# Optimization experiments

Hardware: AMD Instinct MI355X
Metric: run time of the kernel (lower is better)

Reference implementation:

```python
import jax, jax.numpy as jnp
import numpy as np

N_NODES = 100000
N_EDGES = 1600000
IN_C = 64
HID = 64
OUT_C = 40


def setup_inputs() -> dict:
    key = jax.random.key(0)
    ks = jax.random.split(key, 12)
    def lin_init(k, fan_in, shape):
        bound = 1.0 / np.sqrt(fan_in)
        return jax.random.uniform(k, shape, jnp.float32, -bound, bound)
    x0 = jax.random.normal(ks[0], (N_NODES, IN_C), jnp.float32)
    edge_index = jax.random.randint(ks[1], (2, N_EDGES), 0, N_NODES, jnp.int64)
    return {
        "x0": x0,
        "edge_index": edge_index,
        "W1": lin_init(ks[2], IN_C, (HID, IN_C)),
        "b1": lin_init(ks[3], IN_C, (HID,)),
        "Wr1": lin_init(ks[4], IN_C, (HID, IN_C)),
        "br1": lin_init(ks[5], IN_C, (HID,)),
        "W2": lin_init(ks[6], HID, (HID, HID)),
        "b2": lin_init(ks[7], HID, (HID,)),
        "Wr2": lin_init(ks[8], HID, (HID, HID)),
        "br2": lin_init(ks[9], HID, (HID,)),
        "Wl": lin_init(ks[10], 2 * HID, (OUT_C, 2 * HID)),
        "bl": lin_init(ks[11], 2 * HID, (OUT_C,)),
    }


def _norm_weights(row, col, num_nodes):
    # symmetric degree normalization: d^-1/2[row] * d^-1/2[col]
    ones = jnp.ones(row.shape[0], jnp.float32)
    deg = jax.ops.segment_sum(ones, row, num_segments=num_nodes)
    dis = jnp.where(deg > 0, jax.lax.rsqrt(jnp.maximum(deg, 1.0)) * jnp.where(deg > 0, 1.0, 0.0), 0.0)
    dis = jnp.where(deg > 0, deg ** -0.5, 0.0)
    return dis[row] * dis[col]


def _bigraph_conv(x, row, col, w, W, b, Wr, br, num_nodes):
    h = x @ W.T + b                                    # [N, out]
    msg = w[:, None] * h[col]                          # gather + scale, [E, out]
    agg = jax.ops.segment_sum(msg, row, num_segments=num_nodes)
    return agg + x @ Wr.T + br


def reference(x0, edge_index, W1, b1, Wr1, br1, W2, b2, Wr2, br2, Wl, bl):
    num_nodes = x0.shape[0]
    row, col = edge_index[0], edge_index[1]
    w = _norm_weights(row, col, num_nodes)
    x1 = jax.nn.relu(_bigraph_conv(x0, row, col, w, W1, b1, Wr1, br1, num_nodes))
    x2 = jax.nn.relu(_bigraph_conv(x1, row, col, w, W2, b2, Wr2, br2, num_nodes))
    x = jnp.concatenate([x1, x2], axis=-1)
    logits = x @ Wl.T + bl
    return jax.nn.log_softmax(logits, axis=-1)
```

## Files before the change

### kernel.cpp

```cpp
#include <hip/hip_runtime.h>
#include <math.h>


typedef unsigned short u16;
typedef unsigned int   u32;

#define BROWS 512
#define BIN_CHUNK 8192
#define CAPB 12288

__device__ __forceinline__ u16 f2bf(float f) {
  u32 u = __float_as_uint(f);
  u32 r = u + 0x7fffu + ((u >> 16) & 1u);
  return (u16)(r >> 16);
}
__device__ __forceinline__ float bf2f(u16 h) {
  return __uint_as_float(((u32)h) << 16);
}

__global__ __launch_bounds__(1024) void k_binA(
    const int* __restrict__ row, const int* __restrict__ col,
    unsigned* __restrict__ bCnt, unsigned* __restrict__ pairs,
    int nE, int NB, int capA)
{
  __shared__ unsigned buf[BIN_CHUNK];
  __shared__ unsigned cnt[16][256];
  __shared__ unsigned base[256], gb[256], tot[256], sc[256];
  const int t = threadIdx.x;
  const int wave = t >> 6, lane = t & 63;
  const int tb = blockIdx.x * BIN_CHUNK;

  for (int i = t; i < 16 * 256; i += 1024) ((unsigned*)cnt)[i] = 0;
  __syncthreads();

  unsigned pk[8];
  unsigned short po[8];
  short bk[8];
#pragma unroll
  for (int j = 0; j < 8; ++j) {
    int i = tb + j * 1024 + t;
    if (i < nE) {
      int r = row[i], c = col[i];
      int b = r >> 9;
      pk[j] = ((unsigned)(r & (BROWS - 1)) << 17) | (unsigned)c;
      bk[j] = (short)b;
      po[j] = (unsigned short)atomicAdd(&cnt[wave][b], 1u);
    } else bk[j] = -1;
  }
  __syncthreads();

  if (t < 256) {
    unsigned run = 0;
#pragma unroll
    for (int w = 0; w < 16; ++w) {
      unsigned c = cnt[w][t];
      cnt[w][t] = run;
      run += c;
    }
    tot[t] = run;
    sc[t] = run;
  }
  __syncthreads();
  for (int off = 1; off < 256; off <<= 1) {
    unsigned v = 0;
    if (t < 256 && t >= off) v = sc[t - off];
    __syncthreads();
    if (t < 256) sc[t] += v;
    __syncthreads();
  }
  if (t < 256) {
    base[t] = t ? sc[t - 1] : 0u;
    unsigned c = tot[t];
    gb[t] = c ? atomicAdd(&bCnt[t], c) : 0u;
  }
  __syncthreads();

#pragma unroll
  for (int j = 0; j < 8; ++j)
    if (bk[j] >= 0) buf[base[bk[j]] + cnt[wave][bk[j]] + po[j]] = pk[j];
  __syncthreads();

  for (int b = wave; b < NB; b += 16) {
    unsigned cb = tot[b];
    if (!cb) continue;
    unsigned lo = base[b], g = gb[b];
    size_t dst = (size_t)b * (unsigned)capA;
    for (unsigned u = lane; u < cb; u += 64)
      if (g + u < (unsigned)capA) pairs[dst + g + u] = buf[lo + u];
  }
}

__global__ __launch_bounds__(256) void k_bscan(const unsigned* __restrict__ bCnt,
                                               unsigned* __restrict__ bBase, int NB) {
  __shared__ unsigned sc[256];
  int t = threadIdx.x;
  unsigned v = (t < NB) ? min(bCnt[t], (unsigned)CAPB) : 0u;
  sc[t] = v;
  __syncthreads();
  for (int off = 1; off < 256; off <<= 1) {
    unsigned u = (t >= off) ? sc[t - off] : 0u;
    __syncthreads();
    sc[t] += u;
    __syncthreads();
  }
  if (t < NB) bBase[t] = t ? sc[t - 1] : 0u;
}

__global__ __launch_bounds__(512) void k_binB(
    const unsigned* __restrict__ pairs, const unsigned* __restrict__ bCnt,
    const unsigned* __restrict__ bBase, int* __restrict__ colS,
    unsigned* __restrict__ start, float* __restrict__ dis,
    int N, int capA)
{
  __shared__ unsigned hist[BROWS], cur[BROWS], sc[BROWS];
  __shared__ unsigned cols[CAPB];
  const int t = threadIdx.x;
  const int b = blockIdx.x;
  const unsigned cnt = min(bCnt[b], (unsigned)CAPB);
  const unsigned gbase = bBase[b];
  const size_t src = (size_t)b * (unsigned)capA;

  hist[t] = 0;
  __syncthreads();
  for (unsigned i = t; i < cnt; i += 512)
    atomicAdd(&hist[pairs[src + i] >> 17], 1u);
  __syncthreads();
  const unsigned h = hist[t];
  sc[t] = h;
  __syncthreads();
  for (int off = 1; off < 512; off <<= 1) {
    unsigned v = (t >= off) ? sc[t - off] : 0u;
    __syncthreads();
    sc[t] += v;
    __syncthreads();
  }
  const unsigned e = sc[t] - h;
  cur[t] = e;
  __syncthreads();
  for (unsigned i = t; i < cnt; i += 512) {
    unsigned p = pairs[src + i];
    unsigned pos = atomicAdd(&cur[p >> 17], 1u);
    cols[pos] = p & 0x1FFFFu;
  }
  __syncthreads();
  for (unsigned i = t; i < cnt; i += 512)
    colS[gbase + i] = (int)cols[i];
  const int n = b * BROWS + t;
  if (n < N) {
    start[n] = gbase + e + h;
    dis[n] = h ? rsqrtf((float)h) : 0.f;
  }
}

__global__ __launch_bounds__(256) void k_deg(const int* __restrict__ row,
                                             unsigned* __restrict__ deg, int nE) {
  int i = blockIdx.x * blockDim.x + threadIdx.x;
  int stride = gridDim.x * blockDim.x;
  for (; i < nE; i += stride) atomicAdd(&deg[row[i]], 1u);
}

__global__ __launch_bounds__(256) void k_dis(const unsigned* __restrict__ deg,
                                             float* __restrict__ dis, int n) {
  int i = blockIdx.x * blockDim.x + threadIdx.x;
  if (i < n) {
    unsigned d = deg[i];
    dis[i] = d > 0u ? rsqrtf((float)d) : 0.f;
  }
}

__global__ __launch_bounds__(256) void k_scan1(const unsigned* __restrict__ deg,
                                               unsigned* __restrict__ start,
                                               unsigned* __restrict__ bsum, int n) {
  __shared__ unsigned s[256];
  const int base = blockIdx.x * 2048;
  unsigned v[8], tsum = 0;
#pragma unroll
  for (int j = 0; j < 8; ++j) {
    int idx = base + threadIdx.x * 8 + j;
    v[j] = idx < n ? deg[idx] : 0u;
    tsum += v[j];
  }
  s[threadIdx.x] = tsum;
  __syncthreads();
  for (int off = 1; off < 256; off <<= 1) {
    unsigned t = (threadIdx.x >= off) ? s[threadIdx.x - off] : 0u;
    __syncthreads();
    s[threadIdx.x] += t;
    __syncthreads();
  }
  unsigned run = threadIdx.x ? s[threadIdx.x - 1] : 0u;
  if (threadIdx.x == 255) bsum[blockIdx.x] = s[255];
#pragma unroll
  for (int j = 0; j < 8; ++j) {
    int idx = base + threadIdx.x * 8 + j;
    if (idx < n) start[idx] = run;
    run += v[j];
  }
}

__global__ void k_scan2(unsigned* __restrict__ bsum, int nB) {
  if (threadIdx.x == 0 && blockIdx.x == 0) {
    unsigned run = 0;
    for (int b = 0; b < nB; ++b) { unsigned t = bsum[b]; bsum[b] = run; run += t; }
  }
}

__global__ __launch_bounds__(256) void k_scan3(unsigned* __restrict__ start,
                                               const unsigned* __restrict__ bsum, int n) {
  int i = blockIdx.x * blockDim.x + threadIdx.x;
  if (i < n) start[i] += bsum[i >> 11];
}

__global__ __launch_bounds__(256) void k_build(const int* __restrict__ row,
                                               const int* __restrict__ col,
                                               unsigned* __restrict__ start,
                                               int* __restrict__ colS, int nE) {
  int i = blockIdx.x * blockDim.x + threadIdx.x;
  int stride = gridDim.x * blockDim.x;
  for (; i < nE; i += stride) {
    int r = row[i];
    unsigned p = atomicAdd(&start[r], 1u);
    colS[p] = col[i];
  }
}

__global__ __launch_bounds__(256) void k_wgt(
    const int* __restrict__ colS, const unsigned* __restrict__ startEnd,
    const float* __restrict__ dis, uint2* __restrict__ rec,
    float* __restrict__ rs, int nNodes)
{
  const int t = threadIdx.x;
  const int sub = t & 15;
  const int n = blockIdx.x * 16 + (t >> 4);
  if (n >= nNodes) return;
  const unsigned lo = n ? startEnd[n - 1] : 0u;
  const unsigned hi = startEnd[n];
  float s = 0.f;
  for (unsigned u = lo + sub; u < hi; u += 16) {
    int c = colS[u];
    float w = dis[c];
    rec[u] = make_uint2((unsigned)c, __float_as_uint(w));
    s += w;
  }
  s += __shfl_xor(s, 1); s += __shfl_xor(s, 2);
  s += __shfl_xor(s, 4); s += __shfl_xor(s, 8);
  if (sub == 0) rs[n] = dis[n] * s;
}

__global__ __launch_bounds__(256) void k_cast(const float4* __restrict__ x4,
                                              ushort4* __restrict__ out, int n4) {
  int i = blockIdx.x * blockDim.x + threadIdx.x;
  int stride = gridDim.x * blockDim.x;
  for (; i < n4; i += stride) {
    float4 f = x4[i];
    ushort4 v;
    v.x = f2bf(f.x); v.y = f2bf(f.y); v.z = f2bf(f.z); v.w = f2bf(f.w);
    out[i] = v;
  }
}

__global__ __launch_bounds__(256) void k_prep(
    const float* __restrict__ W1, const float* __restrict__ b1,
    const float* __restrict__ Wr1, const float* __restrict__ br1,
    const float* __restrict__ W2, const float* __restrict__ b2,
    const float* __restrict__ Wr2, const float* __restrict__ br2,
    float4* __restrict__ UT)
{
  int i = blockIdx.x * 256 + threadIdx.x;
  if (i >= 2 * 33 * 64) return;
  int layer = i / (33 * 64);
  int kq = (i / 64) % 33;
  int o = i % 64;
  const float* W  = layer ? W2  : W1;
  const float* Wr = layer ? Wr2 : Wr1;
  const float* b  = layer ? b2  : b1;
  const float* br = layer ? br2 : br1;
  float4 v;
  if (kq < 16)       v = ((const float4*)W)[o * 16 + kq];
  else if (kq < 32)  v = ((const float4*)Wr)[o * 16 + kq - 16];
  else               v = make_float4(b[o], br[o], 0.f, 0.f);
  UT[i] = v;
}

__global__ __launch_bounds__(256) void k_spmm_rec(
    const u16* __restrict__ xh, u16* __restrict__ aggh,
    const uint2* __restrict__ rec, const unsigned* __restrict__ startEnd,
    const float* __restrict__ dis, int nNodes)
{
  const int t = threadIdx.x;
  const int sub = t & 15;
  const int n = blockIdx.x * 16 + (t >> 4);
  if (n >= nNodes) return;
  const unsigned lo = n ? startEnd[n - 1] : 0u;
  const unsigned hi = startEnd[n];
  const ushort4* h4 = (const ushort4*)xh;

  float ax = 0.f, ay = 0.f, az = 0.f, aw = 0.f;
  unsigned p = lo;
  for (; p + 4 <= hi; p += 4) {
    uint2 r0 = rec[p],     r1 = rec[p + 1];
    uint2 r2 = rec[p + 2], r3 = rec[p + 3];
    ushort4 v0 = h4[(size_t)r0.x * 16 + sub];
    ushort4 v1 = h4[(size_t)r1.x * 16 + sub];
    ushort4 v2 = h4[(size_t)r2.x * 16 + sub];
    ushort4 v3 = h4[(size_t)r3.x * 16 + sub];
    float w0 = __uint_as_float(r0.y), w1 = __uint_as_float(r1.y);
    float w2 = __uint_as_float(r2.y), w3 = __uint_as_float(r3.y);
    ax += w0 * bf2f(v0.x) + w1 * bf2f(v1.x) + w2 * bf2f(v2.x) + w3 * bf2f(v3.x);
    ay += w0 * bf2f(v0.y) + w1 * bf2f(v1.y) + w2 * bf2f(v2.y) + w3 * bf2f(v3.y);
    az += w0 * bf2f(v0.z) + w1 * bf2f(v1.z) + w2 * bf2f(v2.z) + w3 * bf2f(v3.z);
    aw += w0 * bf2f(v0.w) + w1 * bf2f(v1.w) + w2 * bf2f(v2.w) + w3 * bf2f(v3.w);
  }
  for (; p < hi; ++p) {
    uint2 r = rec[p];
    ushort4 v = h4[(size_t)r.x * 16 + sub];
    float w = __uint_as_float(r.y);
    ax += w * bf2f(v.x); ay += w * bf2f(v.y);
    az += w * bf2f(v.z); aw += w * bf2f(v.w);
  }
  const float dn = dis[n];
  ushort4 o;
  o.x = f2bf(dn * ax); o.y = f2bf(dn * ay);
  o.z = f2bf(dn * az); o.w = f2bf(dn * aw);
  ((ushort4*)aggh)[(size_t)n * 16 + sub] = o;
}

__global__ __launch_bounds__(256) void k_gemv(
    const u16* __restrict__ aggh, const float* __restrict__ rs,
    const u16* __restrict__ rooth, const float4* __restrict__ UT,
    u16* __restrict__ xo, int nNodes)
{
  __shared__ u16 xsh[64][136];
  const int t = threadIdx.x;
  const int lane = t & 63;
  const int og = __builtin_amdgcn_readfirstlane(t >> 6);
  const int n0 = blockIdx.x * 64;

  {
    const int r = t >> 2, q = t & 3;
    int gn = n0 + r; if (gn > nNodes - 1) gn = nNodes - 1;
    const uint4* a = (const uint4*)(aggh + (size_t)gn * 64);
    const uint4* x = (const uint4*)(rooth + (size_t)gn * 64);
    *(uint4*)&xsh[r][q * 16]           = a[q * 2];
    *(uint4*)&xsh[r][q * 16 + 8]       = a[q * 2 + 1];
    *(uint4*)&xsh[r][64 + q * 16]      = x[q * 2];
    *(uint4*)&xsh[r][64 + q * 16 + 8]  = x[q * 2 + 1];
  }
  __syncthreads();

  float acc[16];
#pragma unroll
  for (int j = 0; j < 16; ++j) acc[j] = 0.f;

#pragma unroll 4
  for (int k = 0; k < 32; ++k) {
    ushort4 v = *(const ushort4*)&xsh[lane][k * 4];
    float xa = bf2f(v.x), xb = bf2f(v.y), xc = bf2f(v.z), xd = bf2f(v.w);
    const float4* w = UT + k * 64 + og * 16;
#pragma unroll
    for (int j = 0; j < 16; ++j) {
      float4 W = w[j];
      acc[j] = fmaf(xa, W.x, fmaf(xb, W.y, fmaf(xc, W.z, fmaf(xd, W.w, acc[j]))));
    }
  }

  const int n = n0 + lane;
  const float rsv = (n < nNodes) ? rs[n] : 0.f;
  {
    const float4* w = UT + 32 * 64 + og * 16;
#pragma unroll
    for (int j = 0; j < 16; ++j) {
      float4 W = w[j];
      acc[j] = fmaf(rsv, W.x, acc[j]) + W.y;
    }
  }

  if (n < nNodes) {
    uint4 u0, u1;
    u0.x = (u32)f2bf(fmaxf(acc[0], 0.f))  | ((u32)f2bf(fmaxf(acc[1], 0.f)) << 16);
    u0.y = (u32)f2bf(fmaxf(acc[2], 0.f))  | ((u32)f2bf(fmaxf(acc[3], 0.f)) << 16);
    u0.z = (u32)f2bf(fmaxf(acc[4], 0.f))  | ((u32)f2bf(fmaxf(acc[5], 0.f)) << 16);
    u0.w = (u32)f2bf(fmaxf(acc[6], 0.f))  | ((u32)f2bf(fmaxf(acc[7], 0.f)) << 16);
    u1.x = (u32)f2bf(fmaxf(acc[8], 0.f))  | ((u32)f2bf(fmaxf(acc[9], 0.f)) << 16);
    u1.y = (u32)f2bf(fmaxf(acc[10], 0.f)) | ((u32)f2bf(fmaxf(acc[11], 0.f)) << 16);
    u1.z = (u32)f2bf(fmaxf(acc[12], 0.f)) | ((u32)f2bf(fmaxf(acc[13], 0.f)) << 16);
    u1.w = (u32)f2bf(fmaxf(acc[14], 0.f)) | ((u32)f2bf(fmaxf(acc[15], 0.f)) << 16);
    uint4* dst = (uint4*)(xo + (size_t)n * 64 + og * 16);
    dst[0] = u0;
    dst[1] = u1;
  }
}

__global__ __launch_bounds__(256) void k_final(
    const u16* __restrict__ x1h, const u16* __restrict__ x2h,
    const float* __restrict__ Wl, const float* __restrict__ bl,
    float* __restrict__ out, int nNodes)
{
  __shared__ float4 xs[64][33];
  __shared__ float redM[64][4];
  __shared__ float redS[64][4];
  const int t = threadIdx.x;
  const int lane = t & 63;
  const int og = __builtin_amdgcn_readfirstlane(t >> 6);
  const int nodeBase = blockIdx.x * 64;

  {
    const int sn = t >> 2, q = t & 3;
    int gn = nodeBase + sn;
    if (gn > nNodes - 1) gn = nNodes - 1;
    const ushort4* a = (q < 2) ? (const ushort4*)(x1h + (size_t)gn * 64)
                               : (const ushort4*)(x2h + (size_t)gn * 64);
    const int qq = q & 1;
#pragma unroll
    for (int j = 0; j < 8; ++j) {
      ushort4 v = a[qq * 8 + j];
      xs[sn][q * 8 + j] = make_float4(bf2f(v.x), bf2f(v.y), bf2f(v.z), bf2f(v.w));
    }
  }
  __syncthreads();

  const float4* W4 = (const float4*)Wl;
  float acc[10];
#pragma unroll
  for (int j = 0; j < 10; ++j) acc[j] = bl[og * 10 + j];
  for (int k = 0; k < 32; ++k) {
    float4 x = xs[lane][k];
#pragma unroll
    for (int j = 0; j < 10; ++j) {
      float4 w = W4[(og * 10 + j) * 32 + k];
      acc[j] += w.x * x.x + w.y * x.y + w.z * x.z + w.w * x.w;
    }
  }

  float m10 = acc[0];
#pragma unroll
  for (int j = 1; j < 10; ++j) m10 = fmaxf(m10, acc[j]);
  redM[lane][og] = m10;
  __syncthreads();
  float M = fmaxf(fmaxf(redM[lane][0], redM[lane][1]),
                  fmaxf(redM[lane][2], redM[lane][3]));
  float s10 = 0.f;
#pragma unroll
  for (int j = 0; j < 10; ++j) s10 += __expf(acc[j] - M);
  redS[lane][og] = s10;
  __syncthreads();
  const float S = redS[lane][0] + redS[lane][1] + redS[lane][2] + redS[lane][3];
  const float lse = M + __logf(S);

  const int n = nodeBase + lane;
  if (n < nNodes) {
    float2* o2 = (float2*)(out + (size_t)n * 40 + og * 10);
#pragma unroll
    for (int q = 0; q < 5; ++q)
      o2[q] = make_float2(acc[2 * q] - lse, acc[2 * q + 1] - lse);
  }
}

extern "C" void kernel_launch(void* const* d_in, const int* in_sizes, int n_in,
                              void* d_out, int out_size, void* d_ws, size_t ws_size,
                              hipStream_t stream) {
  const float* x0  = (const float*)d_in[0];
  const int*   ei  = (const int*)d_in[1];
  const float* W1  = (const float*)d_in[2];
  const float* b1  = (const float*)d_in[3];
  const float* Wr1 = (const float*)d_in[4];
  const float* br1 = (const float*)d_in[5];
  const float* W2  = (const float*)d_in[6];
  const float* b2  = (const float*)d_in[7];
  const float* Wr2 = (const float*)d_in[8];
  const float* br2 = (const float*)d_in[9];
  const float* Wl  = (const float*)d_in[10];
  const float* bl  = (const float*)d_in[11];
  float* out = (float*)d_out;

  const int N = in_sizes[0] / 64;
  const int E = in_sizes[1] / 2;
  const int* row = ei;
  const int* col = ei + E;

  const int NB = (N + BROWS - 1) / BROWS;
  const int capA = 16384;
  const int avg = E / (NB > 0 ? NB : 1);
  const bool binOK = (N <= 131072) && (NB <= 256) &&
                     (avg + 12 * (int)sqrtf((float)avg + 1.f) + 256 <= CAPB);

  size_t P = (size_t)NB * capA;
  if (P < (size_t)32 * N) P = (size_t)32 * N;

  const size_t UT_W = 2 * 33 * 64 * 4;
  const size_t needBin = 4 * (512 + P + (size_t)3 * E + (size_t)3 * N + UT_W +
                              (size_t)32 * N + (size_t)32 * N);
  const size_t needCSR = 4 * ((size_t)4 * N + 64 + (size_t)3 * E + UT_W +
                              (size_t)32 * N + (size_t)32 * N + (size_t)32 * N);

  unsigned *start = nullptr; float *dis = nullptr, *rsv = nullptr;
  int* colS = nullptr; uint2* rec = nullptr; float4* UT = nullptr;
  u16 *aggh = nullptr, *x0h = nullptr, *x1h = nullptr, *x2h = nullptr;
  bool ok = false;

  if (binOK && ws_size >= needBin) {
    unsigned* bCnt  = (unsigned*)d_ws;
    unsigned* bBase = bCnt + 256;
    unsigned* pairs = bBase + 256;
    colS  = (int*)(pairs + P);
    rec   = (uint2*)(colS + E);
    start = (unsigned*)(rec + E);
    dis   = (float*)(start + N);
    rsv   = dis + N;
    UT    = (float4*)(rsv + N);
    aggh  = (u16*)(UT + 2 * 33 * 64);
    x1h   = aggh + (size_t)64 * N;
    x0h   = (u16*)pairs;
    x2h   = (u16*)pairs;

    hipMemsetAsync(bCnt, 0, 256 * 4, stream);
    k_binA<<<(E + BIN_CHUNK - 1) / BIN_CHUNK, 1024, 0, stream>>>(row, col, bCnt, pairs, E, NB, capA);
    k_bscan<<<1, 256, 0, stream>>>(bCnt, bBase, NB);
    k_binB<<<NB, 512, 0, stream>>>(pairs, bCnt, bBase, colS, start, dis, N, capA);
    ok = true;
  } else if (ws_size >= needCSR) {
    unsigned* deg = (unsigned*)d_ws;
    start = deg + N;
    dis   = (float*)(start + N);
    rsv   = dis + N;
    unsigned* bsum = (unsigned*)(rsv + N);
    colS  = (int*)(bsum + 64);
    rec   = (uint2*)(colS + E);
    UT    = (float4*)(rec + E);
    aggh  = (u16*)(UT + 2 * 33 * 64);
    x1h   = aggh + (size_t)64 * N;
    u16* xsh = x1h + (size_t)64 * N;
    x0h = xsh; x2h = xsh;

    const int nB = (N + 2047) / 2048;
    hipMemsetAsync(deg, 0, (size_t)N * 4, stream);
    k_deg<<<1024, 256, 0, stream>>>(row, deg, E);
    k_dis<<<(N + 255) / 256, 256, 0, stream>>>(deg, dis, N);
    k_scan1<<<nB, 256, 0, stream>>>(deg, start, bsum, N);
    k_scan2<<<1, 64, 0, stream>>>(bsum, nB);
    k_scan3<<<(N + 255) / 256, 256, 0, stream>>>(start, bsum, N);
    k_build<<<1024, 256, 0, stream>>>(row, col, start, colS, E);
    ok = true;
  }

  if (!ok) return;

  k_wgt<<<(N + 15) / 16, 256, 0, stream>>>(colS, start, dis, rec, rsv, N);
  k_cast<<<1024, 256, 0, stream>>>((const float4*)x0, (ushort4*)x0h, N * 16);
  k_prep<<<17, 256, 0, stream>>>(W1, b1, Wr1, br1, W2, b2, Wr2, br2, UT);

  k_spmm_rec<<<(N + 15) / 16, 256, 0, stream>>>(x0h, aggh, rec, start, dis, N);
  k_gemv<<<(N + 63) / 64, 256, 0, stream>>>(aggh, rsv, x0h, UT, x1h, N);

  k_spmm_rec<<<(N + 15) / 16, 256, 0, stream>>>(x1h, aggh, rec, start, dis, N);
  k_gemv<<<(N + 63) / 64, 256, 0, stream>>>(aggh, rsv, x1h, UT + 33 * 64, x2h, N);

  k_final<<<(N + 63) / 64, 256, 0, stream>>>(x1h, x2h, Wl, bl, out, N);
}
```

Measured before the change: 225.1 us.

## Sort nodes by degree for balanced SpMM wavefronts and unroll gather by eight

Adds a degree histogram, scan and placement pass that builds a permutation grouping nodes of similar degree. The weight and SpMM kernels then process nodes in that order, so the 16-lane groups sharing a wavefront have similar loop trip counts and less divergence. The SpMM inner loop also gains an 8-way unrolled stage for more loads in flight. The cost is three extra small kernels, a memset, and an indirection through perm that scatters the aggh writes and loses the locality of rec reads within a block.

```diff
diff --git a/kernel.cpp b/kernel.cpp
--- a/kernel.cpp
+++ b/kernel.cpp
@@ -224,15 +224,55 @@
   }
 }
 
+__global__ __launch_bounds__(256) void k_dhist(const unsigned* __restrict__ startEnd,
+                                               unsigned* __restrict__ dcnt, int N) {
+  __shared__ unsigned h[64];
+  if (threadIdx.x < 64) h[threadIdx.x] = 0;
+  __syncthreads();
+  int i = blockIdx.x * blockDim.x + threadIdx.x;
+  int stride = gridDim.x * blockDim.x;
+  for (; i < N; i += stride) {
+    unsigned d = startEnd[i] - (i ? startEnd[i - 1] : 0u);
+    atomicAdd(&h[min(d, 63u)], 1u);
+  }
+  __syncthreads();
+  if (threadIdx.x < 64 && h[threadIdx.x]) atomicAdd(&dcnt[threadIdx.x], h[threadIdx.x]);
+}
+
+__global__ void k_dscan(const unsigned* __restrict__ dcnt,
+                        unsigned* __restrict__ dbase) {
+  int t = threadIdx.x;
+  unsigned c = dcnt[t];
+  unsigned v = c;
+  for (int off = 1; off < 64; off <<= 1) {
+    unsigned u = __shfl_up(v, off);
+    if (t >= off) v += u;
+  }
+  dbase[t] = v - c;
+}
+
+__global__ __launch_bounds__(256) void k_dplace(const unsigned* __restrict__ startEnd,
+                                                unsigned* __restrict__ dbase,
+                                                int* __restrict__ perm, int N) {
+  int i = blockIdx.x * blockDim.x + threadIdx.x;
+  int stride = gridDim.x * blockDim.x;
+  for (; i < N; i += stride) {
+    unsigned d = startEnd[i] - (i ? startEnd[i - 1] : 0u);
+    unsigned pos = atomicAdd(&dbase[min(d, 63u)], 1u);
+    perm[pos] = i;
+  }
+}
+
 __global__ __launch_bounds__(256) void k_wgt(
     const int* __restrict__ colS, const unsigned* __restrict__ startEnd,
-    const float* __restrict__ dis, uint2* __restrict__ rec,
-    float* __restrict__ rs, int nNodes)
+    const float* __restrict__ dis, const int* __restrict__ perm,
+    uint2* __restrict__ rec, float* __restrict__ rs, int nNodes)
 {
   const int t = threadIdx.x;
   const int sub = t & 15;
-  const int n = blockIdx.x * 16 + (t >> 4);
-  if (n >= nNodes) return;
+  const int idx = blockIdx.x * 16 + (t >> 4);
+  if (idx >= nNodes) return;
+  const int n = perm[idx];
   const unsigned lo = n ? startEnd[n - 1] : 0u;
   const unsigned hi = startEnd[n];
   float s = 0.f;
@@ -285,18 +325,45 @@
 __global__ __launch_bounds__(256) void k_spmm_rec(
     const u16* __restrict__ xh, u16* __restrict__ aggh,
     const uint2* __restrict__ rec, const unsigned* __restrict__ startEnd,
-    const float* __restrict__ dis, int nNodes)
+    const float* __restrict__ dis, const int* __restrict__ perm, int nNodes)
 {
   const int t = threadIdx.x;
   const int sub = t & 15;
-  const int n = blockIdx.x * 16 + (t >> 4);
-  if (n >= nNodes) return;
+  const int idx = blockIdx.x * 16 + (t >> 4);
+  if (idx >= nNodes) return;
+  const int n = perm[idx];
   const unsigned lo = n ? startEnd[n - 1] : 0u;
   const unsigned hi = startEnd[n];
   const ushort4* h4 = (const ushort4*)xh;
 
   float ax = 0.f, ay = 0.f, az = 0.f, aw = 0.f;
   unsigned p = lo;
+  for (; p + 8 <= hi; p += 8) {
+    uint2 r0 = rec[p],     r1 = rec[p + 1];
+    uint2 r2 = rec[p + 2], r3 = rec[p + 3];
+    uint2 r4 = rec[p + 4], r5 = rec[p + 5];
+    uint2 r6 = rec[p + 6], r7 = rec[p + 7];
+    ushort4 v0 = h4[(size_t)r0.x * 16 + sub];
+    ushort4 v1 = h4[(size_t)r1.x * 16 + sub];
+    ushort4 v2 = h4[(size_t)r2.x * 16 + sub];
+    ushort4 v3 = h4[(size_t)r3.x * 16 + sub];
+    ushort4 v4 = h4[(size_t)r4.x * 16 + sub];
+    ushort4 v5 = h4[(size_t)r5.x * 16 + sub];
+    ushort4 v6 = h4[(size_t)r6.x * 16 + sub];
+    ushort4 v7 = h4[(size_t)r7.x * 16 + sub];
+    float w0 = __uint_as_float(r0.y), w1 = __uint_as_float(r1.y);
+    float w2 = __uint_as_float(r2.y), w3 = __uint_as_float(r3.y);
+    float w4 = __uint_as_float(r4.y), w5 = __uint_as_float(r5.y);
+    float w6 = __uint_as_float(r6.y), w7 = __uint_as_float(r7.y);
+    ax += w0 * bf2f(v0.x) + w1 * bf2f(v1.x) + w2 * bf2f(v2.x) + w3 * bf2f(v3.x);
+    ay += w0 * bf2f(v0.y) + w1 * bf2f(v1.y) + w2 * bf2f(v2.y) + w3 * bf2f(v3.y);
+    az += w0 * bf2f(v0.z) + w1 * bf2f(v1.z) + w2 * bf2f(v2.z) + w3 * bf2f(v3.z);
+    aw += w0 * bf2f(v0.w) + w1 * bf2f(v1.w) + w2 * bf2f(v2.w) + w3 * bf2f(v3.w);
+    ax += w4 * bf2f(v4.x) + w5 * bf2f(v5.x) + w6 * bf2f(v6.x) + w7 * bf2f(v7.x);
+    ay += w4 * bf2f(v4.y) + w5 * bf2f(v5.y) + w6 * bf2f(v6.y) + w7 * bf2f(v7.y);
+    az += w4 * bf2f(v4.z) + w5 * bf2f(v5.z) + w6 * bf2f(v6.z) + w7 * bf2f(v7.z);
+    aw += w4 * bf2f(v4.w) + w5 * bf2f(v5.w) + w6 * bf2f(v6.w) + w7 * bf2f(v7.w);
+  }
   for (; p + 4 <= hi; p += 4) {
     uint2 r0 = rec[p],     r1 = rec[p + 1];
     uint2 r2 = rec[p + 2], r3 = rec[p + 3];
@@ -488,13 +555,14 @@
   if (P < (size_t)32 * N) P = (size_t)32 * N;
 
   const size_t UT_W = 2 * 33 * 64 * 4;
-  const size_t needBin = 4 * (512 + P + (size_t)3 * E + (size_t)3 * N + UT_W +
+  const size_t needBin = 4 * (640 + P + (size_t)3 * E + (size_t)4 * N + UT_W +
                               (size_t)32 * N + (size_t)32 * N);
-  const size_t needCSR = 4 * ((size_t)4 * N + 64 + (size_t)3 * E + UT_W +
+  const size_t needCSR = 4 * ((size_t)5 * N + 192 + (size_t)3 * E + UT_W +
                               (size_t)32 * N + (size_t)32 * N + (size_t)32 * N);
 
   unsigned *start = nullptr; float *dis = nullptr, *rsv = nullptr;
-  int* colS = nullptr; uint2* rec = nullptr; float4* UT = nullptr;
+  int *colS = nullptr, *perm = nullptr; uint2* rec = nullptr; float4* UT = nullptr;
+  unsigned *dcnt = nullptr, *dbase = nullptr;
   u16 *aggh = nullptr, *x0h = nullptr, *x1h = nullptr, *x2h = nullptr;
   bool ok = false;
 
@@ -507,13 +575,17 @@
     start = (unsigned*)(rec + E);
     dis   = (float*)(start + N);
     rsv   = dis + N;
-    UT    = (float4*)(rsv + N);
+    dcnt  = (unsigned*)(rsv + N);
+    dbase = dcnt + 64;
+    perm  = (int*)(dbase + 64);
+    UT    = (float4*)(perm + N);
     aggh  = (u16*)(UT + 2 * 33 * 64);
     x1h   = aggh + (size_t)64 * N;
     x0h   = (u16*)pairs;
     x2h   = (u16*)pairs;
 
     hipMemsetAsync(bCnt, 0, 256 * 4, stream);
+    hipMemsetAsync(dcnt, 0, 64 * 4, stream);
     k_binA<<<(E + BIN_CHUNK - 1) / BIN_CHUNK, 1024, 0, stream>>>(row, col, bCnt, pairs, E, NB, capA);
     k_bscan<<<1, 256, 0, stream>>>(bCnt, bBase, NB);
     k_binB<<<NB, 512, 0, stream>>>(pairs, bCnt, bBase, colS, start, dis, N, capA);
@@ -524,7 +596,10 @@
     dis   = (float*)(start + N);
     rsv   = dis + N;
     unsigned* bsum = (unsigned*)(rsv + N);
-    colS  = (int*)(bsum + 64);
+    dcnt  = bsum + 64;
+    dbase = dcnt + 64;
+    perm  = (int*)(dbase + 64);
+    colS  = (int*)(perm + N);
     rec   = (uint2*)(colS + E);
     UT    = (float4*)(rec + E);
     aggh  = (u16*)(UT + 2 * 33 * 64);
@@ -534,6 +609,7 @@
 
     const int nB = (N + 2047) / 2048;
     hipMemsetAsync(deg, 0, (size_t)N * 4, stream);
+    hipMemsetAsync(dcnt, 0, 64 * 4, stream);
     k_deg<<<1024, 256, 0, stream>>>(row, deg, E);
     k_dis<<<(N + 255) / 256, 256, 0, stream>>>(deg, dis, N);
     k_scan1<<<nB, 256, 0, stream>>>(deg, start, bsum, N);
@@ -545,14 +621,18 @@
 
   if (!ok) return;
 
-  k_wgt<<<(N + 15) / 16, 256, 0, stream>>>(colS, start, dis, rec, rsv, N);
+  k_dhist<<<512, 256, 0, stream>>>(start, dcnt, N);
+  k_dscan<<<1, 64, 0, stream>>>(dcnt, dbase);
+  k_dplace<<<512, 256, 0, stream>>>(start, dbase, perm, N);
+
+  k_wgt<<<(N + 15) / 16, 256, 0, stream>>>(colS, start, dis, perm, rec, rsv, N);
   k_cast<<<1024, 256, 0, stream>>>((const float4*)x0, (ushort4*)x0h, N * 16);
   k_prep<<<17, 256, 0, stream>>>(W1, b1, Wr1, br1, W2, b2, Wr2, br2, UT);
 
-  k_spmm_rec<<<(N + 15) / 16, 256, 0, stream>>>(x0h, aggh, rec, start, dis, N);
+  k_spmm_rec<<<(N + 15) / 16, 256, 0, stream>>>(x0h, aggh, rec, start, dis, perm, N);
   k_gemv<<<(N + 63) / 64, 256, 0, stream>>>(aggh, rsv, x0h, UT, x1h, N);
 
-  k_spmm_rec<<<(N + 15) / 16, 256, 0, stream>>>(x1h, aggh, rec, start, dis, N);
+  k_spmm_rec<<<(N + 15) / 16, 256, 0, stream>>>(x1h, aggh, rec, start, dis, perm, N);
   k_gemv<<<(N + 63) / 64, 256, 0, stream>>>(aggh, rsv, x1h, UT + 33 * 64, x2h, N);
 
   k_final<<<(N + 63) / 64, 256, 0, stream>>>(x1h, x2h, Wl, bl, out, N);
```

Measured after the change: 494.8 us. 2.2x slower.
